# Kernel tuning notes

Hardware: AMD Instinct MI355X
Metric: run time of the kernel (lower is better)

## Reference

```python
import jax, jax.numpy as jnp
import numpy as np

CIN = (512, 1024, 512, 256, 256, 256)
S = (64, 32, 16, 8, 4, 2)
P = 7  # corr_size
B = 8
CH = [P * P + c // 8 for c in CIN]  # lstm state channels per level


def conv3x3(x, w, b):
    y = jax.lax.conv_general_dilated(x, w, (1, 1), ((1, 1), (1, 1)),
                                     dimension_numbers=('NCHW', 'OIHW', 'NCHW'))
    return y + b[None, :, None, None]


def spatial_corr(f1, f2, patch=P):
    # corr[b, di*patch+dj, y, x] = sum_c f1[b,c,y,x] * f2[b,c, y+di-r, x+dj-r]
    r = patch // 2
    Bn, C, H, W = f1.shape
    f2p = jnp.pad(f2, ((0, 0), (0, 0), (r, r), (r, r)))
    outs = [jnp.sum(f1 * f2p[:, :, di:di + H, dj:dj + W], axis=1)
            for di in range(patch) for dj in range(patch)]
    return jnp.stack(outs, axis=1)  # (B, patch*patch, H, W)


def setup_inputs() -> dict:
    key = jax.random.key(0)
    ks = iter(jax.random.split(key, 200))
    d = {}
    for i, (c, s) in enumerate(zip(CIN, S)):
        ch = CH[i]
        d[f'x{i}'] = jax.random.normal(next(ks), (B, c, s, s), jnp.float32)
        d[f'xp{i}'] = jax.random.normal(next(ks), (B, c, s, s), jnp.float32)
        d[f'h{i}'] = jax.random.normal(next(ks), (B, ch, s, s), jnp.float32)
        d[f'c{i}'] = jax.random.normal(next(ks), (B, ch, s, s), jnp.float32)
        d[f'sw{i}'] = jax.random.normal(next(ks), (c // 8, c, 3, 3), jnp.float32) / np.sqrt(c * 9.0)
        d[f'sb{i}'] = jnp.zeros((c // 8,), jnp.float32)
        d[f'lw{i}'] = jax.random.normal(next(ks), (4 * ch, 2 * ch, 3, 3), jnp.float32) / np.sqrt(2 * ch * 9.0)
        d[f'lb{i}'] = jnp.zeros((4 * ch,), jnp.float32)
    return d


def _forward(xs, xps, hs, cs, sws, sbs, lws, lbs):
    h_next, c_next, corrs = [], [], []
    for i in range(len(CIN)):
        summary = jax.nn.relu(conv3x3(xs[i], sws[i], sbs[i]))            # (B, C/8, s, s)
        cf = jax.nn.leaky_relu(spatial_corr(xs[i], xps[i]), 0.01)        # (B, P*P, s, s)
        corrs.append(cf)
        lstm_in = jnp.concatenate([summary, cf, hs[i]], axis=1)          # (B, 2*ch, s, s)
        cx = conv3x3(lstm_in, lws[i], lbs[i])                            # (B, 4*ch, s, s)
        ci, cfg, co, cg = jnp.split(cx, 4, axis=1)
        ig = jax.nn.sigmoid(ci)
        fg = jax.nn.sigmoid(cfg)
        og = jax.nn.sigmoid(co)
        gg = jnp.tanh(cg)
        cn = fg * cs[i] + ig * gg
        hn = og * jnp.tanh(cn)
        h_next.append(hn)
        c_next.append(cn)
    return tuple(h_next + c_next + corrs)


def reference(x0, x1, x2, x3, x4, x5,
              xp0, xp1, xp2, xp3, xp4, xp5,
              h0, h1, h2, h3, h4, h5,
              c0, c1, c2, c3, c4, c5,
              sw0, sw1, sw2, sw3, sw4, sw5,
              sb0, sb1, sb2, sb3, sb4, sb5,
              lw0, lw1, lw2, lw3, lw4, lw5,
              lb0, lb1, lb2, lb3, lb4, lb5):
    xs = [x0, x1, x2, x3, x4, x5]
    xps = [xp0, xp1, xp2, xp3, xp4, xp5]
    hs = [h0, h1, h2, h3, h4, h5]
    cs = [c0, c1, c2, c3, c4, c5]
    sws = [sw0, sw1, sw2, sw3, sw4, sw5]
    sbs = [sb0, sb1, sb2, sb3, sb4, sb5]
    lws = [lw0, lw1, lw2, lw3, lw4, lw5]
    lbs = [lb0, lb1, lb2, lb3, lb4, lb5]
    return _forward(xs, xps, hs, cs, sws, sbs, lws, lbs)
```

## Files before the change

### kernel.cpp

```cpp
#include <hip/hip_runtime.h>
#include <math.h>

typedef _Float16 f16;
typedef _Float16 f16x8 __attribute__((ext_vector_type(8)));
typedef float f32x4 __attribute__((ext_vector_type(4)));

__device__ __forceinline__ float sigmoidf_(float x) { return 1.0f / (1.0f + expf(-x)); }

#define NB 8

__device__ __forceinline__ void decode_swz(int p, int Mtiles, int& mtile, int& nt) {
  if ((Mtiles & 7) == 0) {
    int mch = Mtiles >> 3;
    int c = p & 7, inner = p >> 3;
    nt = inner / mch;
    mtile = c * mch + (inner - nt * mch);
  } else {
    mtile = p % Mtiles;
    nt = p / Mtiles;
  }
}

__global__ void k_nchw2nhwc(const float* __restrict__ in, f16* __restrict__ out,
                            int C, int S, int Cpad, int coff, int Wp, int pad) {
  __shared__ float tile[16][17];
  int xt = blockIdx.x;
  int ct = blockIdx.y;
  int by = blockIdx.z;
  int b = by / S, y = by % S;
  int x0 = xt * 16, c0 = ct * 16;
  int tx = threadIdx.x & 15, tc = threadIdx.x >> 4;
  float v = 0.f;
  if (c0 + tc < C && x0 + tx < S)
    v = in[(((size_t)b * C + c0 + tc) * S + y) * S + x0 + tx];
  tile[tc][tx] = v;
  __syncthreads();
  int tcc = threadIdx.x & 15;
  int txx = threadIdx.x >> 4;
  if (c0 + tcc < C && x0 + txx < S) {
    int c = coff + c0 + tcc;
    out[((((size_t)b * (Cpad >> 5) + (c >> 5)) * Wp + (y + pad)) * Wp + (x0 + txx + pad)) * 32
        + (c & 31)] = (f16)tile[tcc][txx];
  }
}

__global__ void k_wlstm(const float* __restrict__ w, f16* __restrict__ wt,
                        int CH, int CH2, int Jpad, int Cpad) {
  int idx = blockIdx.x * blockDim.x + threadIdx.x;
  int JB16 = Jpad >> 4, KBL = Cpad >> 5;
  int total = 9 * 4 * JB16 * KBL * 512;
  if (idx >= total) return;
  int e = idx & 31;
  int jj = (idx >> 5) & 15;
  int t = idx >> 9;
  int cb = t % KBL; t /= KBL;
  int jb = t % JB16; t /= JB16;
  int g = t & 3; int kk = t >> 2;
  int j = jb * 16 + jj, ci = cb * 32 + e;
  float v = 0.f;
  if (j < CH && ci < CH2)
    v = w[((size_t)(g * CH + j) * CH2 + ci) * 9 + kk];
  wt[idx] = (f16)v;
}

__global__ void k_wsum(const float* __restrict__ w, f16* __restrict__ wt,
                       int C8, int C, int Npad, int Cpad) {
  int idx = blockIdx.x * blockDim.x + threadIdx.x;
  int NB16 = Npad >> 4, KBX = Cpad >> 5;
  int total = 9 * NB16 * KBX * 512;
  if (idx >= total) return;
  int e = idx & 31;
  int nn = (idx >> 5) & 15;
  int t = idx >> 9;
  int cb = t % KBX; t /= KBX;
  int nb = t % NB16; int kk = t / NB16;
  int co = nb * 16 + nn, ci = cb * 32 + e;
  float v = 0.f;
  if (co < C8 && ci < C)
    v = w[((size_t)co * C + ci) * 9 + kk];
  wt[idx] = (f16)v;
}

__global__ void __launch_bounds__(256)
k_conv_gemm(const f16* __restrict__ A,
            const f16* __restrict__ Wt,
            const float* __restrict__ bias,
            f16* __restrict__ D,
            int S, int lS, int CpadX, int CpadL, int C8, int Npad, int M) {
  int w = threadIdx.x >> 6;
  int lane = threadIdx.x & 63;
  int quad = lane >> 4, r = lane & 15;
  int KBX = CpadX >> 5, KBL = CpadL >> 5, NB16 = Npad >> 4;
  int Mt = (M + 127) >> 7;
  int mtile, ntile;
  decode_swz(blockIdx.x, Mt, mtile, ntile);
  int nb0 = ntile * 4;
  int Sp = S + 2;
  size_t pbase[2];
#pragma unroll
  for (int s = 0; s < 2; s++) {
    int m = mtile * 128 + w * 32 + s * 16 + r;
    if (m >= M) m = M - 1;
    int b = m >> (2 * lS);
    int rem = m & ((1 << (2 * lS)) - 1);
    int y = rem >> lS, x = rem & ((1 << lS) - 1);
    pbase[s] = (((size_t)b * KBX * Sp + y) * Sp + x) * 32 + quad * 8;
  }
  size_t wlane = ((size_t)r << 5) + quad * 8;
  size_t tstep = ((size_t)KBX) << 9;
  f32x4 acc[2][4] = {};
  int T = 9 * KBX;
  int cb = 0, kk = 0;

#define CG_LOAD(AF, BF) do { \
    int ky_ = kk / 3, kx_ = kk - 3 * ky_; \
    size_t aoff_ = ((size_t)cb * Sp * Sp + ky_ * Sp + kx_) * 32; \
    size_t wb_ = (((size_t)(kk * NB16 + nb0) * KBX + cb) << 9) + wlane; \
    AF[0] = *(const f16x8*)(A + pbase[0] + aoff_); \
    AF[1] = *(const f16x8*)(A + pbase[1] + aoff_); \
    _Pragma("unroll") for (int t_ = 0; t_ < 4; t_++) \
      BF[t_] = *(const f16x8*)(Wt + wb_ + (size_t)t_ * tstep); \
  } while (0)
#define CG_ADV() do { kk++; if (kk == 9) { kk = 0; cb++; } } while (0)
#define CG_MF(AF, BF) do { \
    _Pragma("unroll") for (int s_ = 0; s_ < 2; s_++) \
    _Pragma("unroll") for (int t_ = 0; t_ < 4; t_++) \
      acc[s_][t_] = __builtin_amdgcn_mfma_f32_16x16x32_f16(AF[s_], BF[t_], acc[s_][t_], 0, 0, 0); \
  } while (0)

  {
    f16x8 a0[2], b0[4], a1[2], b1[4];
    CG_LOAD(a0, b0); CG_ADV();
    int rem = T - 1;
    while (rem >= 2) {
      CG_LOAD(a1, b1); CG_ADV();
      CG_MF(a0, b0);
      CG_LOAD(a0, b0); CG_ADV();
      CG_MF(a1, b1);
      rem -= 2;
    }
    if (rem == 1) { CG_LOAD(a1, b1); CG_MF(a0, b0); CG_MF(a1, b1); }
    else { CG_MF(a0, b0); }
  }
#undef CG_LOAD
#undef CG_ADV
#undef CG_MF

#pragma unroll
  for (int s = 0; s < 2; s++) {
#pragma unroll
    for (int i = 0; i < 4; i++) {
      int m = mtile * 128 + w * 32 + s * 16 + quad * 4 + i;
      if (m >= M) continue;
      int b = m >> (2 * lS);
      int rem = m & ((1 << (2 * lS)) - 1);
      int y = rem >> lS, x = rem & ((1 << lS) - 1);
#pragma unroll
      for (int t = 0; t < 4; t++) {
        int co = (nb0 + t) * 16 + r;
        if (co < C8) {
          float v = acc[s][t][i] + bias[co];
          D[((((size_t)b * KBL + (co >> 5)) * Sp + (y + 1)) * Sp + (x + 1)) * 32 + (co & 31)]
              = (f16)fmaxf(v, 0.f);
        }
      }
    }
  }
}

__global__ void __launch_bounds__(256)
k_lstm_gemm(const f16* __restrict__ A,
            const f16* __restrict__ Wt,
            const float* __restrict__ lb,
            const float* __restrict__ cprev,
            float* __restrict__ hout, float* __restrict__ cout,
            int S, int lS, int CpadL, int CH, int Jpad, int M) {
  int w = threadIdx.x >> 6;
  int lane = threadIdx.x & 63;
  int quad = lane >> 4, r = lane & 15;
  int KBL = CpadL >> 5, JB16 = Jpad >> 4;
  int Mt = (M + 127) >> 7;
  int mtile, jt;
  decode_swz(blockIdx.x, Mt, mtile, jt);
  int Sp = S + 2;
  size_t pbase[2];
#pragma unroll
  for (int s = 0; s < 2; s++) {
    int m = mtile * 128 + w * 32 + s * 16 + r;
    if (m >= M) m = M - 1;
    int b = m >> (2 * lS);
    int rem = m & ((1 << (2 * lS)) - 1);
    int y = rem >> lS, x = rem & ((1 << lS) - 1);
    pbase[s] = (((size_t)b * KBL * Sp + y) * Sp + x) * 32 + quad * 8;
  }
  size_t wlane = ((size_t)r << 5) + quad * 8;
  size_t gstep = ((size_t)JB16 * KBL) << 9;
  f32x4 acc[2][4] = {};
  int T = 9 * KBL;
  int cb = 0, kk = 0;

#define LG_LOAD(AF, BF) do { \
    int ky_ = kk / 3, kx_ = kk - 3 * ky_; \
    size_t aoff_ = ((size_t)cb * Sp * Sp + ky_ * Sp + kx_) * 32; \
    size_t wb_ = (((size_t)(kk * 4 * JB16 + jt) * KBL + cb) << 9) + wlane; \
    AF[0] = *(const f16x8*)(A + pbase[0] + aoff_); \
    AF[1] = *(const f16x8*)(A + pbase[1] + aoff_); \
    _Pragma("unroll") for (int g_ = 0; g_ < 4; g_++) \
      BF[g_] = *(const f16x8*)(Wt + wb_ + (size_t)g_ * gstep); \
  } while (0)
#define LG_ADV() do { kk++; if (kk == 9) { kk = 0; cb++; } } while (0)
#define LG_MF(AF, BF) do { \
    _Pragma("unroll") for (int s_ = 0; s_ < 2; s_++) \
    _Pragma("unroll") for (int g_ = 0; g_ < 4; g_++) \
      acc[s_][g_] = __builtin_amdgcn_mfma_f32_16x16x32_f16(AF[s_], BF[g_], acc[s_][g_], 0, 0, 0); \
  } while (0)

  {
    f16x8 a0[2], b0[4], a1[2], b1[4];
    LG_LOAD(a0, b0); LG_ADV();
    int rem = T - 1;
    while (rem >= 2) {
      LG_LOAD(a1, b1); LG_ADV();
      LG_MF(a0, b0);
      LG_LOAD(a0, b0); LG_ADV();
      LG_MF(a1, b1);
      rem -= 2;
    }
    if (rem == 1) { LG_LOAD(a1, b1); LG_MF(a0, b0); LG_MF(a1, b1); }
    else { LG_MF(a0, b0); }
  }
#undef LG_LOAD
#undef LG_ADV
#undef LG_MF

  int j = jt * 16 + r;
  if (j >= CH) return;
  float bi = lb[j];
  float bf_ = lb[CH + j];
  float bo = lb[2 * CH + j];
  float bg = lb[3 * CH + j];
#pragma unroll
  for (int s = 0; s < 2; s++) {
#pragma unroll
    for (int i = 0; i < 4; i++) {
      int m = mtile * 128 + w * 32 + s * 16 + quad * 4 + i;
      if (m >= M) continue;
      int b = m >> (2 * lS);
      int rem = m & ((1 << (2 * lS)) - 1);
      int y = rem >> lS, x = rem & ((1 << lS) - 1);
      size_t o = (((size_t)b * CH + j) * S + y) * S + x;
      float ig = sigmoidf_(acc[s][0][i] + bi);
      float fg = sigmoidf_(acc[s][1][i] + bf_);
      float og = sigmoidf_(acc[s][2][i] + bo);
      float gg = tanhf(acc[s][3][i] + bg);
      float cn = fg * cprev[o] + ig * gg;
      hout[o] = og * tanhf(cn);
      cout[o] = cn;
    }
  }
}

__global__ void k_corr(const float* __restrict__ f1, const float* __restrict__ f2,
                       float* __restrict__ corr_out, f16* __restrict__ D,
                       int C, int S, int CpadL, int C8) {
  int idx = blockIdx.x * blockDim.x + threadIdx.x;
  int total = NB * 49 * S * S;
  if (idx >= total) return;
  int px = idx % S; int t = idx / S;
  int py = t % S; t /= S;
  int d = t % 49; int b = t / 49;
  int qy = py + d / 7 - 3;
  int qx = px + d % 7 - 3;

  float acc = 0.f;
  if (qy >= 0 && qy < S && qx >= 0 && qx < S) {
    const float* p1 = f1 + ((size_t)b * C * S + py) * S + px;
    const float* p2 = f2 + ((size_t)b * C * S + qy) * S + qx;
    size_t cs = (size_t)S * S;
    for (int ci = 0; ci < C; ci++) {
      acc += p1[(size_t)ci * cs] * p2[(size_t)ci * cs];
    }
  }
  float lr = (acc > 0.f) ? acc : 0.01f * acc;
  corr_out[idx] = lr;
  int Sp = S + 2;
  int ch = C8 + d, KBL = CpadL >> 5;
  D[((((size_t)b * KBL + (ch >> 5)) * Sp + (py + 1)) * Sp + (px + 1)) * 32 + (ch & 31)] = (f16)lr;
}

template<int S>
__global__ void __launch_bounds__(256)
k_corr_mfma(const f16* __restrict__ A,
            const f16* __restrict__ A2,
            float* __restrict__ corr_out,
            f16* __restrict__ D,
            int C, int CpadL, int C8) {
  constexpr int XT = S / 16;
  constexpr int Sp = S + 2, Sq = S + 6;
  int KBX = C >> 5, KBL = CpadL >> 5;
  int nb = gridDim.x;
  int eb = (blockIdx.x % 8) * (nb / 8) + blockIdx.x / 8;
  int wid = eb * 4 + (threadIdx.x >> 6);
  int lane = threadIdx.x & 63;
  int quad = lane >> 4, r = lane & 15;
  int xt = wid % XT; int t1 = wid / XT;
  int y = t1 % S; int b = t1 / S;
  int x0 = xt * 16;

  size_t baseA = ((((size_t)b * KBX) * Sp + (y + 1)) * Sp + (x0 + r + 1)) * 32 + quad * 8;
  size_t stepA = (size_t)Sp * Sp * 32;
  int xs1 = x0 + 16 + r; if (xs1 > S + 5) xs1 = S + 5;
  size_t off0 = (size_t)(x0 + r) * 32 + quad * 8;
  size_t off1 = (size_t)xs1 * 32 + quad * 8;
  size_t baseB = ((size_t)b * KBX) * Sq * Sq * 32 + (size_t)y * Sq * 32;
  size_t stepB = (size_t)Sq * Sq * 32;

  f32x4 acc[7][2] = {};
  for (int cbi = 0; cbi < KBX; cbi++) {
    f16x8 af = *(const f16x8*)(A + baseA + (size_t)cbi * stepA);
    const f16* pbb = A2 + baseB + (size_t)cbi * stepB;
#pragma unroll
    for (int dyo = 0; dyo < 7; dyo++) {
      const f16* pr = pbb + (size_t)dyo * Sq * 32;
      f16x8 b0 = *(const f16x8*)(pr + off0);
      f16x8 b1 = *(const f16x8*)(pr + off1);
      acc[dyo][0] = __builtin_amdgcn_mfma_f32_16x16x32_f16(af, b0, acc[dyo][0], 0, 0, 0);
      acc[dyo][1] = __builtin_amdgcn_mfma_f32_16x16x32_f16(af, b1, acc[dyo][1], 0, 0, 0);
    }
  }
#pragma unroll
  for (int dyo = 0; dyo < 7; dyo++) {
#pragma unroll
    for (int t = 0; t < 2; t++) {
#pragma unroll
      for (int i = 0; i < 4; i++) {
        int ml = quad * 4 + i;
        int dxo = r - ml + t * 16;
        if (dxo < 0 || dxo > 6) continue;
        float v = acc[dyo][t][i];
        float lr = (v > 0.f) ? v : 0.01f * v;
        int d = dyo * 7 + dxo;
        int x = x0 + ml;
        corr_out[(((size_t)b * 49 + d) * S + y) * S + x] = lr;
        int ch = C8 + d;
        D[((((size_t)b * KBL + (ch >> 5)) * Sp + (y + 1)) * Sp + (x + 1)) * 32 + (ch & 31)]
            = (f16)lr;
      }
    }
  }
}

extern "C" void kernel_launch(void* const* d_in, const int* in_sizes, int n_in,
                              void* d_out, int out_size, void* d_ws, size_t ws_size,
                              hipStream_t stream) {
  (void)in_sizes; (void)n_in; (void)out_size; (void)ws_size;
  static const int CINa[6] = {512, 1024, 512, 256, 256, 256};
  static const int Sa[6]   = {64, 32, 16, 8, 4, 2};
  static const int lSa[6]  = {6, 5, 4, 3, 2, 1};
  static const int CHa[6]  = {113, 177, 113, 81, 81, 81};
  static const int CpadLa[6] = {256, 384, 256, 192, 192, 192};
  static const int Jpada[6]  = {128, 192, 128, 96, 96, 96};
  const int B = 8;

  size_t h_off[6], c_off[6], corr_off[6];
  size_t off = 0;
  for (int i = 0; i < 6; i++) { h_off[i] = off;    off += (size_t)B * CHa[i] * Sa[i] * Sa[i]; }
  for (int i = 0; i < 6; i++) { c_off[i] = off;    off += (size_t)B * CHa[i] * Sa[i] * Sa[i]; }
  for (int i = 0; i < 6; i++) { corr_off[i] = off; off += (size_t)B * 49 * Sa[i] * Sa[i]; }

  float* out = (float*)d_out;
  char* ws = (char*)d_ws;
  const size_t offA = 0;
  const size_t offD = 37748736;
  const size_t offWs = offD + 18874368;
  const size_t offWl = offWs + 3145728;
  const size_t offA2 = offWl + 6291456;

  for (int i = 0; i < 6; i++) {
    const float* x  = (const float*)d_in[8 * i + 0];
    const float* xp = (const float*)d_in[8 * i + 1];
    const float* h  = (const float*)d_in[8 * i + 2];
    const float* c  = (const float*)d_in[8 * i + 3];
    const float* sw = (const float*)d_in[8 * i + 4];
    const float* sb = (const float*)d_in[8 * i + 5];
    const float* lw = (const float*)d_in[8 * i + 6];
    const float* lb = (const float*)d_in[8 * i + 7];
    int C = CINa[i], S = Sa[i], lS = lSa[i], CH = CHa[i], C8 = C / 8;
    int CH2 = 2 * CH, CpadL = CpadLa[i], Jpad = Jpada[i];
    int Sp = S + 2;
    int Npad = (C8 + 63) / 64 * 64;
    int M = B * S * S;
    int Mt128 = (M + 127) / 128;

    f16* Abuf = (f16*)(ws + offA);
    f16* Dbuf = (f16*)(ws + offD);
    f16* Wsum = (f16*)(ws + offWs);
    f16* Wlstm = (f16*)(ws + offWl);
    f16* A2buf = (f16*)(ws + offA2);

    size_t sizeA = (size_t)B * Sp * Sp * C * 2;
    size_t sizeD = (size_t)B * Sp * Sp * CpadL * 2;
    hipMemsetAsync(Abuf, 0, sizeA, stream);
    hipMemsetAsync(Dbuf, 0, sizeD, stream);

    {
      dim3 g((S + 15) / 16, (C + 15) / 16, B * S);
      k_nchw2nhwc<<<g, 256, 0, stream>>>(x, Abuf, C, S, C, 0, Sp, 1);
    }
    {
      int tot = 9 * Npad * C;
      k_wsum<<<(tot + 255) / 256, 256, 0, stream>>>(sw, Wsum, C8, C, Npad, C);
    }
    {
      k_conv_gemm<<<Mt128 * (Npad / 64), 256, 0, stream>>>(Abuf, Wsum, sb, Dbuf,
                                                           S, lS, C, CpadL, C8, Npad, M);
    }
    if (i < 3) {
      int Sq = S + 6;
      size_t sizeA2 = (size_t)B * Sq * Sq * C * 2;
      hipMemsetAsync(A2buf, 0, sizeA2, stream);
      {
        dim3 g((S + 15) / 16, (C + 15) / 16, B * S);
        k_nchw2nhwc<<<g, 256, 0, stream>>>(xp, A2buf, C, S, C, 0, Sq, 3);
      }
      int blocks = B * S * (S / 16) / 4;
      if (i == 0)
        k_corr_mfma<64><<<blocks, 256, 0, stream>>>(Abuf, A2buf, out + corr_off[i], Dbuf,
                                                    C, CpadL, C8);
      else if (i == 1)
        k_corr_mfma<32><<<blocks, 256, 0, stream>>>(Abuf, A2buf, out + corr_off[i], Dbuf,
                                                    C, CpadL, C8);
      else
        k_corr_mfma<16><<<blocks, 256, 0, stream>>>(Abuf, A2buf, out + corr_off[i], Dbuf,
                                                    C, CpadL, C8);
    } else {
      int tot = B * 49 * S * S;
      k_corr<<<(tot + 255) / 256, 256, 0, stream>>>(x, xp, out + corr_off[i], Dbuf,
                                                    C, S, CpadL, C8);
    }
    {
      dim3 g((S + 15) / 16, (CH + 15) / 16, B * S);
      k_nchw2nhwc<<<g, 256, 0, stream>>>(h, Dbuf, CH, S, CpadL, C8 + 49, Sp, 1);
    }
    {
      int tot = 9 * 4 * Jpad * CpadL;
      k_wlstm<<<(tot + 255) / 256, 256, 0, stream>>>(lw, Wlstm, CH, CH2, Jpad, CpadL);
    }
    {
      k_lstm_gemm<<<Mt128 * (Jpad / 16), 256, 0, stream>>>(Dbuf, Wlstm, lb, c,
                                                           out + h_off[i], out + c_off[i],
                                                           S, lS, CpadL, CH, Jpad, M);
    }
  }
}
```

Before: 1.682 ms.

## Stage conv and LSTM GEMM operands through double-buffered LDS with direct global-to-LDS loads

Both the summary-conv GEMM and the LSTM GEMM now copy A and B tiles into a double-buffered shared-memory staging area using global_load_lds. All waves read their MFMA fragments from there, with one barrier per K step. Before, each wave loaded its fragments straight from global memory, so the same weight tiles were fetched redundantly by all four waves. The LSTM kernel also widens its tile to 32 hidden units per block (8 accumulators per row group), which halves the grid and raises weight reuse. In exchange it adds barrier overhead, more registers and fewer blocks. It also assumes Jpad is a multiple of 32.

```diff
diff --git a/kernel.cpp b/kernel.cpp
--- a/kernel.cpp
+++ b/kernel.cpp
@@ -4,6 +4,13 @@
 typedef _Float16 f16;
 typedef _Float16 f16x8 __attribute__((ext_vector_type(8)));
 typedef float f32x4 __attribute__((ext_vector_type(4)));
+
+typedef const void __attribute__((address_space(1))) gvoid;
+typedef void __attribute__((address_space(3))) lvoid;
+
+__device__ __forceinline__ void gl2lds16(const void* g, void* l) {
+  __builtin_amdgcn_global_load_lds((gvoid*)g, (lvoid*)l, 16, 0, 0);
+}
 
 __device__ __forceinline__ float sigmoidf_(float x) { return 1.0f / (1.0f + expf(-x)); }
 
@@ -87,64 +94,63 @@
             const float* __restrict__ bias,
             f16* __restrict__ D,
             int S, int lS, int CpadX, int CpadL, int C8, int Npad, int M) {
-  int w = threadIdx.x >> 6;
-  int lane = threadIdx.x & 63;
-  int quad = lane >> 4, r = lane & 15;
+  __shared__ __attribute__((aligned(16))) f16 ldsA[2][4][128][8];
+  __shared__ __attribute__((aligned(16))) f16 ldsB[2][4][64][8];
+  int t = threadIdx.x;
+  int w = t >> 6, lane = t & 63, quad = lane >> 4, r = lane & 15;
   int KBX = CpadX >> 5, KBL = CpadL >> 5, NB16 = Npad >> 4;
   int Mt = (M + 127) >> 7;
   int mtile, ntile;
   decode_swz(blockIdx.x, Mt, mtile, ntile);
   int nb0 = ntile * 4;
   int Sp = S + 2;
-  size_t pbase[2];
-#pragma unroll
-  for (int s = 0; s < 2; s++) {
-    int m = mtile * 128 + w * 32 + s * 16 + r;
-    if (m >= M) m = M - 1;
-    int b = m >> (2 * lS);
-    int rem = m & ((1 << (2 * lS)) - 1);
+
+  size_t gA;
+  {
+    int m = mtile * 128 + (t & 127); if (m >= M) m = M - 1;
+    int b = m >> (2 * lS); int rem = m & ((1 << (2 * lS)) - 1);
     int y = rem >> lS, x = rem & ((1 << lS) - 1);
-    pbase[s] = (((size_t)b * KBX * Sp + y) * Sp + x) * 32 + quad * 8;
-  }
-  size_t wlane = ((size_t)r << 5) + quad * 8;
-  size_t tstep = ((size_t)KBX) << 9;
+    gA = (((size_t)b * KBX * Sp + y) * Sp + x) * 32 + (size_t)(t >> 7) * 8;
+  }
+  size_t sB = (size_t)((t & 63) >> 4) * ((size_t)KBX << 9)
+              + (size_t)(t & 15) * 32 + (size_t)(t >> 6) * 8;
+  char* lA0 = (char*)&ldsA[0][0][0][0] + t * 16;
+  char* lB0 = (char*)&ldsB[0][0][0][0] + t * 16;
+  int T = 9 * KBX;
+
+#define CSTAGE(buf, it) do { \
+    int cb_ = (it) / 9, kk_ = (it) - 9 * cb_; \
+    int ky_ = kk_ / 3, kx_ = kk_ - 3 * ky_; \
+    const f16* ga_ = A + gA + ((size_t)cb_ * Sp * Sp + ky_ * Sp + kx_) * 32; \
+    const f16* gb_ = Wt + ((((size_t)(kk_ * NB16 + nb0)) * KBX + cb_) << 9) + sB; \
+    char* la_ = lA0 + (buf) * 8192; \
+    gl2lds16(ga_, la_); \
+    gl2lds16(ga_ + 16, la_ + 4096); \
+    gl2lds16(gb_, lB0 + (buf) * 4096); \
+  } while (0)
+
   f32x4 acc[2][4] = {};
-  int T = 9 * KBX;
-  int cb = 0, kk = 0;
-
-#define CG_LOAD(AF, BF) do { \
-    int ky_ = kk / 3, kx_ = kk - 3 * ky_; \
-    size_t aoff_ = ((size_t)cb * Sp * Sp + ky_ * Sp + kx_) * 32; \
-    size_t wb_ = (((size_t)(kk * NB16 + nb0) * KBX + cb) << 9) + wlane; \
-    AF[0] = *(const f16x8*)(A + pbase[0] + aoff_); \
-    AF[1] = *(const f16x8*)(A + pbase[1] + aoff_); \
-    _Pragma("unroll") for (int t_ = 0; t_ < 4; t_++) \
-      BF[t_] = *(const f16x8*)(Wt + wb_ + (size_t)t_ * tstep); \
-  } while (0)
-#define CG_ADV() do { kk++; if (kk == 9) { kk = 0; cb++; } } while (0)
-#define CG_MF(AF, BF) do { \
-    _Pragma("unroll") for (int s_ = 0; s_ < 2; s_++) \
-    _Pragma("unroll") for (int t_ = 0; t_ < 4; t_++) \
-      acc[s_][t_] = __builtin_amdgcn_mfma_f32_16x16x32_f16(AF[s_], BF[t_], acc[s_][t_], 0, 0, 0); \
-  } while (0)
-
-  {
-    f16x8 a0[2], b0[4], a1[2], b1[4];
-    CG_LOAD(a0, b0); CG_ADV();
-    int rem = T - 1;
-    while (rem >= 2) {
-      CG_LOAD(a1, b1); CG_ADV();
-      CG_MF(a0, b0);
-      CG_LOAD(a0, b0); CG_ADV();
-      CG_MF(a1, b1);
-      rem -= 2;
-    }
-    if (rem == 1) { CG_LOAD(a1, b1); CG_MF(a0, b0); CG_MF(a1, b1); }
-    else { CG_MF(a0, b0); }
-  }
-#undef CG_LOAD
-#undef CG_ADV
-#undef CG_MF
+  int cur = 0;
+  CSTAGE(0, 0);
+  __syncthreads();
+  for (int it = 0; it < T; ++it) {
+    if (it + 1 < T) CSTAGE(cur ^ 1, it + 1);
+    f16x8 af[2], bf[4];
+#pragma unroll
+    for (int s = 0; s < 2; s++)
+      af[s] = *(const f16x8*)&ldsA[cur][quad][w * 32 + s * 16 + r][0];
+#pragma unroll
+    for (int q = 0; q < 4; q++)
+      bf[q] = *(const f16x8*)&ldsB[cur][quad][q * 16 + r][0];
+#pragma unroll
+    for (int s = 0; s < 2; s++)
+#pragma unroll
+      for (int q = 0; q < 4; q++)
+        acc[s][q] = __builtin_amdgcn_mfma_f32_16x16x32_f16(af[s], bf[q], acc[s][q], 0, 0, 0);
+    __syncthreads();
+    cur ^= 1;
+  }
+#undef CSTAGE
 
 #pragma unroll
   for (int s = 0; s < 2; s++) {
@@ -156,10 +162,10 @@
       int rem = m & ((1 << (2 * lS)) - 1);
       int y = rem >> lS, x = rem & ((1 << lS) - 1);
 #pragma unroll
-      for (int t = 0; t < 4; t++) {
-        int co = (nb0 + t) * 16 + r;
+      for (int q = 0; q < 4; q++) {
+        int co = (nb0 + q) * 16 + r;
         if (co < C8) {
-          float v = acc[s][t][i] + bias[co];
+          float v = acc[s][q][i] + bias[co];
           D[((((size_t)b * KBL + (co >> 5)) * Sp + (y + 1)) * Sp + (x + 1)) * 32 + (co & 31)]
               = (f16)fmaxf(v, 0.f);
         }
@@ -175,87 +181,94 @@
             const float* __restrict__ cprev,
             float* __restrict__ hout, float* __restrict__ cout,
             int S, int lS, int CpadL, int CH, int Jpad, int M) {
-  int w = threadIdx.x >> 6;
-  int lane = threadIdx.x & 63;
-  int quad = lane >> 4, r = lane & 15;
+  __shared__ __attribute__((aligned(16))) f16 ldsA[2][4][128][8];
+  __shared__ __attribute__((aligned(16))) f16 ldsB[2][4][128][8];
+  int t = threadIdx.x;
+  int w = t >> 6, lane = t & 63, quad = lane >> 4, r = lane & 15;
   int KBL = CpadL >> 5, JB16 = Jpad >> 4;
   int Mt = (M + 127) >> 7;
   int mtile, jt;
   decode_swz(blockIdx.x, Mt, mtile, jt);
   int Sp = S + 2;
-  size_t pbase[2];
-#pragma unroll
-  for (int s = 0; s < 2; s++) {
-    int m = mtile * 128 + w * 32 + s * 16 + r;
-    if (m >= M) m = M - 1;
-    int b = m >> (2 * lS);
-    int rem = m & ((1 << (2 * lS)) - 1);
+
+  size_t gA;
+  {
+    int m = mtile * 128 + (t & 127); if (m >= M) m = M - 1;
+    int b = m >> (2 * lS); int rem = m & ((1 << (2 * lS)) - 1);
     int y = rem >> lS, x = rem & ((1 << lS) - 1);
-    pbase[s] = (((size_t)b * KBL * Sp + y) * Sp + x) * 32 + quad * 8;
-  }
-  size_t wlane = ((size_t)r << 5) + quad * 8;
-  size_t gstep = ((size_t)JB16 * KBL) << 9;
-  f32x4 acc[2][4] = {};
+    gA = (((size_t)b * KBL * Sp + y) * Sp + x) * 32 + (size_t)(t >> 7) * 8;
+  }
+  int nT = t & 127;
+  int gT = nT >> 5, jjT = nT & 31;
+  size_t sB = ((size_t)(gT * JB16 + jt * 2 + (jjT >> 4)) * KBL) * 512
+              + (size_t)(jjT & 15) * 32 + (size_t)(t >> 7) * 8;
+  size_t kkStrB = (size_t)4 * JB16 * KBL * 512;
+  char* lA0 = (char*)&ldsA[0][0][0][0] + t * 16;
+  char* lB0 = (char*)&ldsB[0][0][0][0] + t * 16;
   int T = 9 * KBL;
-  int cb = 0, kk = 0;
-
-#define LG_LOAD(AF, BF) do { \
-    int ky_ = kk / 3, kx_ = kk - 3 * ky_; \
-    size_t aoff_ = ((size_t)cb * Sp * Sp + ky_ * Sp + kx_) * 32; \
-    size_t wb_ = (((size_t)(kk * 4 * JB16 + jt) * KBL + cb) << 9) + wlane; \
-    AF[0] = *(const f16x8*)(A + pbase[0] + aoff_); \
-    AF[1] = *(const f16x8*)(A + pbase[1] + aoff_); \
-    _Pragma("unroll") for (int g_ = 0; g_ < 4; g_++) \
-      BF[g_] = *(const f16x8*)(Wt + wb_ + (size_t)g_ * gstep); \
+
+#define LSTAGE(buf, it) do { \
+    int cb_ = (it) / 9, kk_ = (it) - 9 * cb_; \
+    int ky_ = kk_ / 3, kx_ = kk_ - 3 * ky_; \
+    const f16* ga_ = A + gA + ((size_t)cb_ * Sp * Sp + ky_ * Sp + kx_) * 32; \
+    const f16* gb_ = Wt + (size_t)kk_ * kkStrB + (size_t)cb_ * 512 + sB; \
+    char* la_ = lA0 + (buf) * 8192; \
+    char* lb_ = lB0 + (buf) * 8192; \
+    gl2lds16(ga_, la_); \
+    gl2lds16(ga_ + 16, la_ + 4096); \
+    gl2lds16(gb_, lb_); \
+    gl2lds16(gb_ + 16, lb_ + 4096); \
   } while (0)
-#define LG_ADV() do { kk++; if (kk == 9) { kk = 0; cb++; } } while (0)
-#define LG_MF(AF, BF) do { \
-    _Pragma("unroll") for (int s_ = 0; s_ < 2; s_++) \
-    _Pragma("unroll") for (int g_ = 0; g_ < 4; g_++) \
-      acc[s_][g_] = __builtin_amdgcn_mfma_f32_16x16x32_f16(AF[s_], BF[g_], acc[s_][g_], 0, 0, 0); \
-  } while (0)
-
-  {
-    f16x8 a0[2], b0[4], a1[2], b1[4];
-    LG_LOAD(a0, b0); LG_ADV();
-    int rem = T - 1;
-    while (rem >= 2) {
-      LG_LOAD(a1, b1); LG_ADV();
-      LG_MF(a0, b0);
-      LG_LOAD(a0, b0); LG_ADV();
-      LG_MF(a1, b1);
-      rem -= 2;
-    }
-    if (rem == 1) { LG_LOAD(a1, b1); LG_MF(a0, b0); LG_MF(a1, b1); }
-    else { LG_MF(a0, b0); }
-  }
-#undef LG_LOAD
-#undef LG_ADV
-#undef LG_MF
-
-  int j = jt * 16 + r;
-  if (j >= CH) return;
-  float bi = lb[j];
-  float bf_ = lb[CH + j];
-  float bo = lb[2 * CH + j];
-  float bg = lb[3 * CH + j];
-#pragma unroll
-  for (int s = 0; s < 2; s++) {
-#pragma unroll
-    for (int i = 0; i < 4; i++) {
-      int m = mtile * 128 + w * 32 + s * 16 + quad * 4 + i;
-      if (m >= M) continue;
-      int b = m >> (2 * lS);
-      int rem = m & ((1 << (2 * lS)) - 1);
-      int y = rem >> lS, x = rem & ((1 << lS) - 1);
-      size_t o = (((size_t)b * CH + j) * S + y) * S + x;
-      float ig = sigmoidf_(acc[s][0][i] + bi);
-      float fg = sigmoidf_(acc[s][1][i] + bf_);
-      float og = sigmoidf_(acc[s][2][i] + bo);
-      float gg = tanhf(acc[s][3][i] + bg);
-      float cn = fg * cprev[o] + ig * gg;
-      hout[o] = og * tanhf(cn);
-      cout[o] = cn;
+
+  f32x4 acc[2][8] = {};
+  int cur = 0;
+  LSTAGE(0, 0);
+  __syncthreads();
+  for (int it = 0; it < T; ++it) {
+    if (it + 1 < T) LSTAGE(cur ^ 1, it + 1);
+    f16x8 af[2], bf[8];
+#pragma unroll
+    for (int s = 0; s < 2; s++)
+      af[s] = *(const f16x8*)&ldsA[cur][quad][w * 32 + s * 16 + r][0];
+#pragma unroll
+    for (int q = 0; q < 8; q++)
+      bf[q] = *(const f16x8*)&ldsB[cur][quad][q * 16 + r][0];
+#pragma unroll
+    for (int s = 0; s < 2; s++)
+#pragma unroll
+      for (int q = 0; q < 8; q++)
+        acc[s][q] = __builtin_amdgcn_mfma_f32_16x16x32_f16(af[s], bf[q], acc[s][q], 0, 0, 0);
+    __syncthreads();
+    cur ^= 1;
+  }
+#undef LSTAGE
+
+#pragma unroll
+  for (int jh = 0; jh < 2; jh++) {
+    int j = jt * 32 + jh * 16 + r;
+    if (j >= CH) continue;
+    float bi = lb[j];
+    float bff = lb[CH + j];
+    float bo = lb[2 * CH + j];
+    float bg = lb[3 * CH + j];
+#pragma unroll
+    for (int s = 0; s < 2; s++) {
+#pragma unroll
+      for (int i = 0; i < 4; i++) {
+        int m = mtile * 128 + w * 32 + s * 16 + quad * 4 + i;
+        if (m >= M) continue;
+        int b = m >> (2 * lS);
+        int rem = m & ((1 << (2 * lS)) - 1);
+        int y = rem >> lS, x = rem & ((1 << lS) - 1);
+        size_t o = (((size_t)b * CH + j) * S + y) * S + x;
+        float ig = sigmoidf_(acc[s][0 + jh][i] + bi);
+        float fg = sigmoidf_(acc[s][2 + jh][i] + bff);
+        float og = sigmoidf_(acc[s][4 + jh][i] + bo);
+        float gg = tanhf(acc[s][6 + jh][i] + bg);
+        float cn = fg * cprev[o] + ig * gg;
+        hout[o] = og * tanhf(cn);
+        cout[o] = cn;
+      }
     }
   }
 }
@@ -447,7 +460,7 @@
       k_wlstm<<<(tot + 255) / 256, 256, 0, stream>>>(lw, Wlstm, CH, CH2, Jpad, CpadL);
     }
     {
-      k_lstm_gemm<<<Mt128 * (Jpad / 16), 256, 0, stream>>>(Dbuf, Wlstm, lb, c,
+      k_lstm_gemm<<<Mt128 * (Jpad / 32), 256, 0, stream>>>(Dbuf, Wlstm, lb, c,
                                                            out + h_off[i], out + c_off[i],
                                                            S, lS, CpadL, CH, Jpad, M);
     }
```

Result: slower. 1.888 ms (+12.3%).
